# Kernel optimization log

Measured on AMD Instinct MI355X. Metric: run time of the kernel, lower is better.

The kernel has to match this reference:

```python
import jax, jax.numpy as jnp
import numpy as np

D = 1024
H = 4
HD = D // H
WIN = 128
NPMEM = 4
EPS = 1e-5


def _layernorm(x, g, b):
    mu = jnp.mean(x, axis=-1, keepdims=True)
    var = jnp.var(x, axis=-1, keepdims=True)
    return (x - mu) * jax.lax.rsqrt(var + EPS) * g + b


def _rotate_half(t):
    h = t.shape[-1] // 2
    return jnp.concatenate([-t[..., h:], t[..., :h]], axis=-1)


def setup_inputs() -> dict:
    key = jax.random.key(0)
    ks = jax.random.split(key, 20)
    B, L = 2, 4096
    s = 0.02
    inp = {
        'x': jax.random.normal(ks[0], (B, L, D), jnp.float32),
        'cos': jax.random.uniform(ks[1], (L + 8, HD), jnp.float32),
        'sin': jax.random.uniform(ks[2], (L + 8, HD), jnp.float32),
        'global_out': jax.random.normal(ks[3], (B, L, D), jnp.float32),
        'local_out': jax.random.normal(ks[4], (B, L, D), jnp.float32),
        'wq': jax.random.normal(ks[5], (D, D), jnp.float32) * s,
        'wk': jax.random.normal(ks[6], (D, D), jnp.float32) * s,
        'wv': jax.random.normal(ks[7], (D, D), jnp.float32) * s,
        'wo_attn': jax.random.normal(ks[8], (D, D), jnp.float32) * s,
        'pmem': jax.random.normal(ks[9], (1, NPMEM, D), jnp.float32),
        'gate_w': jax.random.normal(ks[10], (3 * D, 3 * D), jnp.float32) * s,
        'gate_b': jnp.zeros((3 * D,), jnp.float32),
        'outproj_w': jax.random.normal(ks[11], (3 * D, D), jnp.float32) * s,
        'outproj_b': jnp.zeros((D,), jnp.float32),
        'ln_mem_g': jnp.ones((D,), jnp.float32),
        'ln_mem_b': jnp.zeros((D,), jnp.float32),
        'ln_mlp_g': jnp.ones((D,), jnp.float32),
        'ln_mlp_b': jnp.zeros((D,), jnp.float32),
        'fc1_w': jax.random.normal(ks[12], (D, 4 * D), jnp.float32) * s,
        'fc1_b': jnp.zeros((4 * D,), jnp.float32),
        'fc2_w': jax.random.normal(ks[13], (4 * D, D), jnp.float32) * s,
        'fc2_b': jnp.zeros((D,), jnp.float32),
    }
    return inp


def reference(x, cos, sin, global_out, local_out, wq, wk, wv, wo_attn, pmem,
              gate_w, gate_b, outproj_w, outproj_b, ln_mem_g, ln_mem_b,
              ln_mlp_g, ln_mlp_b, fc1_w, fc1_b, fc2_w, fc2_b):
    B, L, _ = x.shape
    residual = x

    # prepend persistent memory tokens
    xp = jnp.concatenate([jnp.broadcast_to(pmem, (B, NPMEM, D)), x], axis=1)
    Lt = L + NPMEM

    q = (xp @ wq).reshape(B, Lt, H, HD)
    k = (xp @ wk).reshape(B, Lt, H, HD)
    v = (xp @ wv).reshape(B, Lt, H, HD)

    # rotary embedding over the full pmem+seq length
    cc = cos[:Lt][None, :, None, :]
    ss = sin[:Lt][None, :, None, :]
    q = q * cc + _rotate_half(q) * ss
    k = k * cc + _rotate_half(k) * ss

    i = jnp.arange(Lt)[:, None]
    j = jnp.arange(Lt)[None, :]
    mask = (j <= i) & (j >= i - WIN)  # [Lt, Lt]

    scale = 1.0 / jnp.sqrt(jnp.asarray(HD, x.dtype))
    scores = jnp.einsum('blhd,bmhd->bhlm', q, k) * scale
    scores = jnp.where(mask[None, None], scores, jnp.finfo(scores.dtype).min)
    attn = jax.nn.softmax(scores, axis=-1)
    out = jnp.einsum('bhlm,bmhd->blhd', attn, v).reshape(B, Lt, D)
    core_out = (out @ wo_attn)[:, -L:, :]

    combined = jnp.concatenate([global_out, local_out, core_out], axis=-1)
    g = jax.nn.sigmoid(combined @ gate_w + gate_b)
    memory_output = (combined * g) @ outproj_w + outproj_b

    x1 = residual + _layernorm(memory_output, ln_mem_g, ln_mem_b)
    xn = _layernorm(x1, ln_mlp_g, ln_mlp_b)
    mlp_out = jax.nn.silu(xn @ fc1_w + fc1_b) @ fc2_w + fc2_b
    return x1 + mlp_out
```

## Files before the change

kernel.cpp:

```cpp
#include <hip/hip_runtime.h>
#include <stdint.h>

#define D_    1024
#define H_    4
#define HD_   256
#define WIN_  128
#define NPM_  4
#define B_    2
#define L_    4096
#define LT_   4100
#define LTP_  4112
#define QKL_  3072

typedef __attribute__((ext_vector_type(8))) short short8;
typedef __attribute__((ext_vector_type(4))) float f32x4;

__device__ __forceinline__ short f2bf(float f) {
  union { float f; uint32_t u; } v; v.f = f;
  uint32_t r = v.u + 0x7FFFu + ((v.u >> 16) & 1u);
  return (short)(r >> 16);
}
__device__ __forceinline__ float bf2f(short h) {
  union { uint32_t u; float f; } v; v.u = ((uint32_t)(uint16_t)h) << 16;
  return v.f;
}

#define EP_BF16 0
#define EP_F32B 1
#define EP_GATE 2
#define EP_SILU 3
#define EP_RES  4
#define EP_CORE 5

template<int EP, int TM>
__global__ __launch_bounds__(256, 2)
void gemm_bt(const short* __restrict__ A, int lda,
             const short* __restrict__ Bt,
             void* __restrict__ Cp, int ldc,
             const float* __restrict__ bias,
             const void* __restrict__ aux, int ldaux,
             int M, int N, int K)
{
  constexpr int WM = TM / 2;
  constexpr int MT = WM / 16;
  constexpr int BUFSZ = (TM + 128) * 32;
  __shared__ __attribute__((aligned(16))) short lds[2 * BUFSZ];
  const int tid  = threadIdx.x;
  const int lane = tid & 63, wave = tid >> 6;
  const int lhi  = lane >> 4, llo = lane & 15;
  const int m0 = blockIdx.x * TM, n0 = blockIdx.y * 128;
  const int mw = (wave >> 1) * WM, nw = (wave & 1) * 64;

  const int srow = tid >> 2;
  const int sg   = (tid & 3) ^ ((tid >> 3) & 3);
  const short* pA0 = A + (size_t)min(m0 + srow, M - 1) * lda + sg * 8;
  const short* pA1 = (TM == 128) ? A + (size_t)min(m0 + srow + 64, M - 1) * lda + sg * 8 : pA0;
  const short* pB0 = Bt + (size_t)(n0 + srow) * K + sg * 8;
  const short* pB1 = Bt + (size_t)(n0 + srow + 64) * K + sg * 8;

  const int segoff = (lhi ^ ((llo >> 1) & 3)) * 8;

  short8 ra0, ra1, rb0, rb1;
  auto loadk = [&](int k) {
    ra0 = *(const short8*)(pA0 + k);
    if constexpr (TM == 128) ra1 = *(const short8*)(pA1 + k);
    rb0 = *(const short8*)(pB0 + k);
    rb1 = *(const short8*)(pB1 + k);
  };
  auto stage = [&](int b) {
    short* base = &lds[b * BUFSZ];
    *(short8*)&base[tid * 8] = ra0;
    if constexpr (TM == 128) *(short8*)&base[2048 + tid * 8] = ra1;
    *(short8*)&base[TM * 32 + tid * 8]        = rb0;
    *(short8*)&base[TM * 32 + 2048 + tid * 8] = rb1;
  };

  f32x4 acc[MT][4];
#pragma unroll
  for (int i = 0; i < MT; i++)
#pragma unroll
    for (int j = 0; j < 4; j++) acc[i][j] = f32x4{0.f, 0.f, 0.f, 0.f};

  const int NI = K >> 5;
  loadk(0);
  stage(0);
  loadk(32);
  __syncthreads();

  for (int i = 0; i < NI; i++) {
    if (i + 1 < NI) stage((i + 1) & 1);
    if (i + 2 < NI) loadk((i + 2) << 5);
    const short* bufp = &lds[(i & 1) * BUFSZ];
    short8 af[MT], bfr[4];
#pragma unroll
    for (int mt = 0; mt < MT; mt++)
      af[mt] = *(const short8*)&bufp[(mw + mt * 16 + llo) * 32 + segoff];
#pragma unroll
    for (int nt = 0; nt < 4; nt++)
      bfr[nt] = *(const short8*)&bufp[TM * 32 + (nw + nt * 16 + llo) * 32 + segoff];
#pragma unroll
    for (int mt = 0; mt < MT; mt++)
#pragma unroll
      for (int nt = 0; nt < 4; nt++)
        acc[mt][nt] = __builtin_amdgcn_mfma_f32_16x16x32_bf16(af[mt], bfr[nt], acc[mt][nt], 0, 0, 0);
    __syncthreads();
  }

  const int gcb = n0 + nw;
#pragma unroll
  for (int mt = 0; mt < MT; mt++) {
    const int gr0 = m0 + mw + mt * 16 + lhi * 4;
#pragma unroll
    for (int nt = 0; nt < 4; nt++) {
      const int gc = gcb + nt * 16 + llo;
      float bv = 0.f;
      if constexpr (EP != EP_BF16 && EP != EP_CORE) bv = bias[gc];
#pragma unroll
      for (int r = 0; r < 4; r++) {
        const int gr = gr0 + r;
        if (gr >= M) continue;
        const float v = acc[mt][nt][r];
        if constexpr (EP == EP_CORE) {
          const int b   = gr >= LT_ ? 1 : 0;
          const int tok = gr - b * LT_;
          if (tok >= NPM_) {
            const int cr = b * L_ + (tok - NPM_);
            ((short*)Cp)[(size_t)cr * ldc + gc] = f2bf(v);
          }
          continue;
        }
        const size_t idx = (size_t)gr * ldc + gc;
        if constexpr (EP == EP_BF16) {
          ((short*)Cp)[idx] = f2bf(v);
        } else if constexpr (EP == EP_F32B) {
          ((float*)Cp)[idx] = v + bv;
        } else if constexpr (EP == EP_GATE) {
          float g  = 1.f / (1.f + __expf(-(v + bv)));
          float cv = bf2f(((const short*)aux)[(size_t)gr * ldaux + gc]);
          ((short*)Cp)[idx] = f2bf(cv * g);
        } else if constexpr (EP == EP_SILU) {
          float xx = v + bv;
          ((short*)Cp)[idx] = f2bf(xx / (1.f + __expf(-xx)));
        } else {
          ((float*)Cp)[idx] = v + bv + ((const float*)aux)[(size_t)gr * ldaux + gc];
        }
      }
    }
  }
}

struct TAll {
  const float* src[8];
  short* dst[8];
  int C[8];
  int R[8];
  int nbx[8];
  int start[8];
};

__global__ __launch_bounds__(256)
void transpose_all(TAll t)
{
  __shared__ short tile[32][33];
  const int bid = blockIdx.x;
  int w = 0;
#pragma unroll
  for (int i = 1; i < 8; i++) w = (bid >= t.start[i]) ? i : w;
  const int rel = bid - t.start[w];
  const int nbx = t.nbx[w];
  const int bx = rel % nbx, by = rel / nbx;
  const float* src = t.src[w];
  short* dst = t.dst[w];
  const int ld_in = t.C[w], ld_out = t.R[w];
  const int r0 = by * 32, c0 = bx * 32;
  const int tx = threadIdx.x & 31, ty = threadIdx.x >> 5;
#pragma unroll
  for (int i = 0; i < 4; i++)
    tile[ty + i * 8][tx] = f2bf(src[(size_t)(r0 + ty + i * 8) * ld_in + c0 + tx]);
  __syncthreads();
#pragma unroll
  for (int i = 0; i < 4; i++)
    dst[(size_t)(c0 + ty + i * 8) * ld_out + r0 + tx] = tile[tx][ty + i * 8];
}

template<typename Tin>
__global__ __launch_bounds__(256)
void cast_transpose(const Tin* __restrict__ in, short* __restrict__ outp,
                    int R, int C, int ld_in, int ld_out,
                    int zdiv, size_t inA, size_t inB, size_t outA, size_t outB)
{
  __shared__ short tile[32][33];
  const int z = blockIdx.z;
  const Tin* src = in + (size_t)(z / zdiv) * inA + (size_t)(z % zdiv) * inB;
  short* dst = outp + (size_t)(z / zdiv) * outA + (size_t)(z % zdiv) * outB;
  const int r0 = blockIdx.y * 32, c0 = blockIdx.x * 32;
  const int tx = threadIdx.x & 31, ty = threadIdx.x >> 5;
#pragma unroll
  for (int i = 0; i < 4; i++) {
    int r = r0 + ty + i * 8, c = c0 + tx;
    short v = 0;
    if (r < R && c < C) {
      if constexpr (sizeof(Tin) == 4) v = f2bf((float)src[(size_t)r * ld_in + c]);
      else                            v = (short)src[(size_t)r * ld_in + c];
    }
    tile[ty + i * 8][tx] = v;
  }
  __syncthreads();
#pragma unroll
  for (int i = 0; i < 4; i++) {
    int c = c0 + ty + i * 8, r = r0 + tx;
    if (c < C && r < R) dst[(size_t)c * ld_out + r] = tile[tx][ty + i * 8];
  }
}

__global__ __launch_bounds__(256)
void build_xp_k(const float* __restrict__ x, const float* __restrict__ pmem,
                short* __restrict__ xp)
{
  int gid = blockIdx.x * 256 + threadIdx.x;
  int row = gid >> 8;
  int c4  = (gid & 255) * 4;
  int b   = row >= LT_ ? 1 : 0;
  int tok = row - b * LT_;
  const float* src = (tok < NPM_) ? (pmem + (size_t)tok * D_ + c4)
                                  : (x + ((size_t)b * L_ + tok - NPM_) * D_ + c4);
  float4 v = *(const float4*)src;
  short o[4] = {f2bf(v.x), f2bf(v.y), f2bf(v.z), f2bf(v.w)};
  *(short4*)&xp[(size_t)row * D_ + c4] = *(short4*)o;
}

__global__ __launch_bounds__(256)
void combined01_k(const float* __restrict__ go, const float* __restrict__ lo,
                  short* __restrict__ comb)
{
  int gid = blockIdx.x * 256 + threadIdx.x;
  int row = gid >> 9;
  int c4  = (gid & 511) * 4;
  const float* src = (c4 < D_) ? (go + (size_t)row * D_ + c4)
                               : (lo + (size_t)row * D_ + (c4 - D_));
  float4 v = *(const float4*)src;
  short o[4] = {f2bf(v.x), f2bf(v.y), f2bf(v.z), f2bf(v.w)};
  *(short4*)&comb[(size_t)row * 3072 + c4] = *(short4*)o;
}

__global__ __launch_bounds__(256)
void rope_kernel(short* __restrict__ qkv,
                 const float* __restrict__ cosp, const float* __restrict__ sinp)
{
  int gid = blockIdx.x * 256 + threadIdx.x;
  int d   = (gid & 31) * 4;
  int h   = (gid >> 5) & 3;
  int row = gid >> 7;
  int t   = row >= LT_ ? row - LT_ : row;
  size_t base = (size_t)row * QKL_ + h * HD_ + d;
  float4 cl = *(const float4*)&cosp[(size_t)t * HD_ + d];
  float4 ch = *(const float4*)&cosp[(size_t)t * HD_ + d + 128];
  float4 sl = *(const float4*)&sinp[(size_t)t * HD_ + d];
  float4 sh = *(const float4*)&sinp[(size_t)t * HD_ + d + 128];
  short4 ql4 = *(const short4*)&qkv[base],        qh4 = *(const short4*)&qkv[base + 128];
  short4 kl4 = *(const short4*)&qkv[base + 1024], kh4 = *(const short4*)&qkv[base + 1152];
  const float SC = 1.f / 16.f;
  short oql[4], oqh[4], okl[4], okh[4];
#pragma unroll
  for (int j = 0; j < 4; j++) {
    float c0 = ((float*)&cl)[j], c1 = ((float*)&ch)[j];
    float s0 = ((float*)&sl)[j], s1 = ((float*)&sh)[j];
    float ql = bf2f(((short*)&ql4)[j]), qh = bf2f(((short*)&qh4)[j]);
    float kl = bf2f(((short*)&kl4)[j]), kh = bf2f(((short*)&kh4)[j]);
    oql[j] = f2bf((ql * c0 - qh * s0) * SC);
    oqh[j] = f2bf((qh * c1 + ql * s1) * SC);
    okl[j] = f2bf(kl * c0 - kh * s0);
    okh[j] = f2bf(kh * c1 + kl * s1);
  }
  *(short4*)&qkv[base]        = *(short4*)oql;
  *(short4*)&qkv[base + 128]  = *(short4*)oqh;
  *(short4*)&qkv[base + 1024] = *(short4*)okl;
  *(short4*)&qkv[base + 1152] = *(short4*)okh;
}

__global__ __launch_bounds__(256, 1)
void attn_kernel(const short* __restrict__ qkv, const short* __restrict__ vT,
                 short* __restrict__ outp)
{
  __shared__ short lKV[256 * 72];
  __shared__ short lP[64 * 200];
  const int tid  = threadIdx.x;
  const int lane = tid & 63, wave = tid >> 6;
  const int lhi  = lane >> 4, llo = lane & 15;
  const int i0 = blockIdx.x * 64;
  const int h = blockIdx.y, b = blockIdx.z;
  const int kw0 = i0 - 128;
  const size_t vbase = (size_t)(b * H_ + h) * HD_ * LTP_;

  short8 qf[8];
  {
    int ic = min(i0 + wave * 16 + llo, LT_ - 1);
    const short* qrow = qkv + (size_t)(b * LT_ + ic) * QKL_ + h * HD_;
#pragma unroll
    for (int ks = 0; ks < 8; ks++)
      qf[ks] = *(const short8*)(qrow + ks * 32 + lhi * 8);
  }

  f32x4 S[12];
#pragma unroll
  for (int st = 0; st < 12; st++) S[st] = f32x4{0.f, 0.f, 0.f, 0.f};

  for (int kc = 0; kc < 3; kc++) {
    if (kc) __syncthreads();
    {
      int row = tid >> 2;
      int jc = min(max(kw0 + kc * 64 + row, 0), LT_ - 1);
      const short* krow = qkv + (size_t)(b * LT_ + jc) * QKL_ + 1024 + h * HD_;
#pragma unroll
      for (int it = 0; it < 8; it++) {
        int seg = (tid & 3) + it * 4;
        *(short8*)&lKV[row * 264 + seg * 8] = *(const short8*)(krow + seg * 8);
      }
    }
    __syncthreads();
#pragma unroll
    for (int ks = 0; ks < 8; ks++) {
#pragma unroll
      for (int nt = 0; nt < 4; nt++) {
        short8 bf = *(const short8*)&lKV[(nt * 16 + llo) * 264 + ks * 32 + lhi * 8];
        S[kc * 4 + nt] = __builtin_amdgcn_mfma_f32_16x16x32_bf16(qf[ks], bf, S[kc * 4 + nt], 0, 0, 0);
      }
    }
  }

  const int irow = i0 + wave * 16 + lhi * 4;
  float mx[4], sm[4];
#pragma unroll
  for (int r = 0; r < 4; r++) mx[r] = -3.0e38f;
#pragma unroll
  for (int st = 0; st < 12; st++) {
    int j = kw0 + st * 16 + llo;
#pragma unroll
    for (int r = 0; r < 4; r++) {
      int i = irow + r;
      bool ok = (j >= 0) & (j <= i) & (j >= i - WIN_);
      float s = ok ? S[st][r] : -1.0e30f;
      S[st][r] = s;
      mx[r] = fmaxf(mx[r], s);
    }
  }
#pragma unroll
  for (int r = 0; r < 4; r++)
#pragma unroll
    for (int o = 1; o < 16; o <<= 1) mx[r] = fmaxf(mx[r], __shfl_xor(mx[r], o));
#pragma unroll
  for (int r = 0; r < 4; r++) sm[r] = 0.f;
#pragma unroll
  for (int st = 0; st < 12; st++)
#pragma unroll
    for (int r = 0; r < 4; r++) {
      float e = __expf(S[st][r] - mx[r]);
      S[st][r] = e;
      sm[r] += e;
    }
#pragma unroll
  for (int r = 0; r < 4; r++) {
#pragma unroll
    for (int o = 1; o < 16; o <<= 1) sm[r] += __shfl_xor(sm[r], o);
    sm[r] = 1.f / sm[r];
  }

#pragma unroll
  for (int st = 0; st < 12; st++)
#pragma unroll
    for (int r = 0; r < 4; r++)
      lP[(wave * 16 + lhi * 4 + r) * 200 + st * 16 + llo] = f2bf(S[st][r] * sm[r]);

  f32x4 O[16];
#pragma unroll
  for (int nt = 0; nt < 16; nt++) O[nt] = f32x4{0.f, 0.f, 0.f, 0.f};

  for (int kc = 0; kc < 3; kc++) {
    __syncthreads();
#pragma unroll
    for (int it = 0; it < 8; it++) {
      int id = it * 256 + tid;
      int d = id >> 3, seg = id & 7;
      int kbase = min(max(kw0 + kc * 64 + seg * 8, 0), LTP_ - 8);
      *(short8*)&lKV[d * 72 + seg * 8] = *(const short8*)&vT[vbase + (size_t)d * LTP_ + kbase];
    }
    __syncthreads();
#pragma unroll
    for (int ks = 0; ks < 2; ks++) {
      short8 pf = *(const short8*)&lP[(wave * 16 + llo) * 200 + kc * 64 + ks * 32 + lhi * 8];
#pragma unroll
      for (int nt = 0; nt < 16; nt++) {
        short8 vf = *(const short8*)&lKV[(nt * 16 + llo) * 72 + ks * 32 + lhi * 8];
        O[nt] = __builtin_amdgcn_mfma_f32_16x16x32_bf16(pf, vf, O[nt], 0, 0, 0);
      }
    }
  }

  short* orow = outp + (size_t)(b * LT_) * D_ + h * HD_;
#pragma unroll
  for (int nt = 0; nt < 16; nt++)
#pragma unroll
    for (int r = 0; r < 4; r++) {
      int i = irow + r;
      if (i < LT_) orow[(size_t)i * D_ + nt * 16 + llo] = f2bf(O[nt][r]);
    }
}

__global__ __launch_bounds__(256, 4)
void ln2_kernel(const float* __restrict__ mo, const float* __restrict__ xres,
                const float* __restrict__ g1, const float* __restrict__ b1,
                const float* __restrict__ g2, const float* __restrict__ b2,
                float* __restrict__ x1, short* __restrict__ xn)
{
  const int row = blockIdx.x;
  const int tid = threadIdx.x;
  const int lane = tid & 63, wave = tid >> 6;
  __shared__ float red[8], red2[8];
  float4 v = ((const float4*)(mo + (size_t)row * D_))[tid];
  float s = v.x + v.y + v.z + v.w;
  float s2 = v.x * v.x + v.y * v.y + v.z * v.z + v.w * v.w;
#pragma unroll
  for (int o = 1; o < 64; o <<= 1) { s += __shfl_xor(s, o); s2 += __shfl_xor(s2, o); }
  if (lane == 0) { red[wave] = s; red[wave + 4] = s2; }
  __syncthreads();
  float S = red[0] + red[1] + red[2] + red[3];
  float S2 = red[4] + red[5] + red[6] + red[7];
  float mu = S * (1.f / D_);
  float rs = rsqrtf(S2 * (1.f / D_) - mu * mu + 1e-5f);
  float4 gg = ((const float4*)g1)[tid];
  float4 bb = ((const float4*)b1)[tid];
  float4 xv = ((const float4*)(xres + (size_t)row * D_))[tid];
  float4 o1;
  o1.x = xv.x + (v.x - mu) * rs * gg.x + bb.x;
  o1.y = xv.y + (v.y - mu) * rs * gg.y + bb.y;
  o1.z = xv.z + (v.z - mu) * rs * gg.z + bb.z;
  o1.w = xv.w + (v.w - mu) * rs * gg.w + bb.w;
  ((float4*)(x1 + (size_t)row * D_))[tid] = o1;
  s = o1.x + o1.y + o1.z + o1.w;
  s2 = o1.x * o1.x + o1.y * o1.y + o1.z * o1.z + o1.w * o1.w;
#pragma unroll
  for (int o = 1; o < 64; o <<= 1) { s += __shfl_xor(s, o); s2 += __shfl_xor(s2, o); }
  if (lane == 0) { red2[wave] = s; red2[wave + 4] = s2; }
  __syncthreads();
  S = red2[0] + red2[1] + red2[2] + red2[3];
  S2 = red2[4] + red2[5] + red2[6] + red2[7];
  float mu2 = S * (1.f / D_);
  float rs2 = rsqrtf(S2 * (1.f / D_) - mu2 * mu2 + 1e-5f);
  float4 g2v = ((const float4*)g2)[tid];
  float4 b2v = ((const float4*)b2)[tid];
  short o2[4];
  o2[0] = f2bf((o1.x - mu2) * rs2 * g2v.x + b2v.x);
  o2[1] = f2bf((o1.y - mu2) * rs2 * g2v.y + b2v.y);
  o2[2] = f2bf((o1.z - mu2) * rs2 * g2v.z + b2v.z);
  o2[3] = f2bf((o1.w - mu2) * rs2 * g2v.w + b2v.w);
  *(short4*)&xn[(size_t)row * D_ + tid * 4] = *(short4*)o2;
}

extern "C" void kernel_launch(void* const* d_in, const int* in_sizes, int n_in,
                              void* d_out, int out_size, void* d_ws, size_t ws_size,
                              hipStream_t stream)
{
  const float* x      = (const float*)d_in[0];
  const float* cosp   = (const float*)d_in[1];
  const float* sinp   = (const float*)d_in[2];
  const float* go     = (const float*)d_in[3];
  const float* lo     = (const float*)d_in[4];
  const float* wq     = (const float*)d_in[5];
  const float* wk     = (const float*)d_in[6];
  const float* wv     = (const float*)d_in[7];
  const float* wo     = (const float*)d_in[8];
  const float* pmem   = (const float*)d_in[9];
  const float* gate_w = (const float*)d_in[10];
  const float* gate_b = (const float*)d_in[11];
  const float* outp_w = (const float*)d_in[12];
  const float* outp_b = (const float*)d_in[13];
  const float* ln1g   = (const float*)d_in[14];
  const float* ln1b   = (const float*)d_in[15];
  const float* ln2g   = (const float*)d_in[16];
  const float* ln2b   = (const float*)d_in[17];
  const float* fc1w   = (const float*)d_in[18];
  const float* fc1b   = (const float*)d_in[19];
  const float* fc2w   = (const float*)d_in[20];
  const float* fc2b   = (const float*)d_in[21];
  float* out = (float*)d_out;
  char* p = (char*)d_ws;

  short* wqkvT = (short*)(p + 0);
  short* woT   = (short*)(p + 6291456);
  short* gateT = (short*)(p + 8388608);
  short* outpT = (short*)(p + 27262976);
  short* fc1T  = (short*)(p + 33554432);
  short* fc2T  = (short*)(p + 41943040);
  short* comb  = (short*)(p + 50331648);
  char*  pool  = p + 100663296;
  short* xp    = (short*)(pool);
  short* qkv   = (short*)(pool + 16793600);
  short* vT    = (short*)(pool + 67174400);
  short* a_o   = (short*)(pool + 84017152);
  short* gated = (short*)(pool);
  short* h1    = (short*)(pool);
  float* mo    = (float*)(pool + 67174400);
  float* x1    = (float*)(comb);
  short* xn    = (short*)((char*)comb + 33554432);

  TAll t;
  const float* srcs[8] = {wq, wk, wv, wo, gate_w, outp_w, fc1w, fc2w};
  short* dsts[8] = {wqkvT, wqkvT + 1048576, wqkvT + 2097152, woT, gateT, outpT, fc1T, fc2T};
  const int Rs[8] = {1024, 1024, 1024, 1024, 3072, 3072, 1024, 4096};
  const int Cs[8] = {1024, 1024, 1024, 1024, 3072, 1024, 4096, 1024};
  int cum = 0;
  for (int i = 0; i < 8; i++) {
    t.src[i] = srcs[i]; t.dst[i] = dsts[i];
    t.R[i] = Rs[i]; t.C[i] = Cs[i]; t.nbx[i] = Cs[i] / 32;
    t.start[i] = cum;
    cum += (Cs[i] / 32) * (Rs[i] / 32);
  }
  transpose_all<<<cum, 256, 0, stream>>>(t);

  build_xp_k<<<8200, 256, 0, stream>>>(x, pmem, xp);
  combined01_k<<<16384, 256, 0, stream>>>(go, lo, comb);

  const int Mq = B_ * LT_;
  gemm_bt<EP_BF16, 128><<<dim3(65, 24), 256, 0, stream>>>(xp, 1024, wqkvT, qkv, QKL_, nullptr, nullptr, 0, Mq, 3072, 1024);

  rope_kernel<<<4100, 256, 0, stream>>>(qkv, cosp, sinp);
  cast_transpose<short><<<dim3(8, 129, 8), 256, 0, stream>>>(
      qkv + 2048, vT, LT_, 256, QKL_, LTP_, 4,
      (size_t)LT_ * QKL_, 256, (size_t)4 * 256 * LTP_, (size_t)256 * LTP_);

  attn_kernel<<<dim3(65, H_, B_), 256, 0, stream>>>(qkv, vT, a_o);

  gemm_bt<EP_CORE, 64><<<dim3(129, 8), 256, 0, stream>>>(
      a_o, 1024, woT, comb + 2048, 3072, nullptr, nullptr, 0, Mq, 1024, 1024);

  gemm_bt<EP_GATE, 128><<<dim3(64, 24), 256, 0, stream>>>(comb, 3072, gateT, gated, 3072, gate_b, comb, 3072, 8192, 3072, 3072);

  gemm_bt<EP_F32B, 64><<<dim3(128, 8), 256, 0, stream>>>(gated, 3072, outpT, mo, 1024, outp_b, nullptr, 0, 8192, 1024, 3072);

  ln2_kernel<<<8192, 256, 0, stream>>>(mo, x, ln1g, ln1b, ln2g, ln2b, x1, xn);

  gemm_bt<EP_SILU, 128><<<dim3(64, 32), 256, 0, stream>>>(xn, 1024, fc1T, h1, 4096, fc1b, nullptr, 0, 8192, 4096, 1024);
  gemm_bt<EP_RES, 64><<<dim3(128, 8), 256, 0, stream>>>(h1, 4096, fc2T, out, 1024, fc2b, x1, 1024, 8192, 1024, 4096);
}
```

Measured before the change: 985.7 us.

## Replace GEMMs with 256x256-tile kernel using direct global-to-LDS loads

```diff
diff --git a/kernel.cpp b/kernel.cpp
--- a/kernel.cpp
+++ b/kernel.cpp
@@ -24,6 +24,16 @@
   union { uint32_t u; float f; } v; v.u = ((uint32_t)(uint16_t)h) << 16;
   return v.f;
 }
+
+typedef __attribute__((address_space(1))) void GAS;
+typedef __attribute__((address_space(3))) void LAS;
+__device__ __forceinline__ void gl16(const void* g, void* l) {
+  __builtin_amdgcn_global_load_lds((GAS*)g, (LAS*)l, 16, 0, 0);
+}
+__device__ __forceinline__ void waitvm8() { asm volatile("s_waitcnt vmcnt(8)" ::: "memory"); }
+__device__ __forceinline__ void waitvm4() { asm volatile("s_waitcnt vmcnt(4)" ::: "memory"); }
+__device__ __forceinline__ void waitvm0() { asm volatile("s_waitcnt vmcnt(0)" ::: "memory"); }
+__device__ __forceinline__ void waitlg0() { asm volatile("s_waitcnt lgkmcnt(0)" ::: "memory"); }
 
 #define EP_BF16 0
 #define EP_F32B 1
@@ -149,6 +159,171 @@
   }
 }
 
+template<int EP>
+__global__ __launch_bounds__(512, 2)
+void gemm_bt256(const short* __restrict__ A,
+                const short* __restrict__ Bt,
+                void* __restrict__ Cp, int ldc,
+                const float* __restrict__ bias,
+                const void* __restrict__ aux, int ldaux,
+                int M, int N, int K)
+{
+  __shared__ __attribute__((aligned(128))) short lds[65536];
+  const int tid  = threadIdx.x;
+  const int lane = tid & 63, wave = tid >> 6;
+  const int llo  = lane & 15, lhi = lane >> 4;
+  const int wm = wave >> 2, wn = wave & 3;
+  const int m0 = blockIdx.x * 256, n0 = blockIdx.y * 256;
+
+  const int s0   = wave * 128 + lane;
+  const int srow = s0 >> 2;
+  const int kd   = ((s0 & 3) ^ (srow & 3) ^ ((srow >> 2) & 3)) * 8;
+  const short* aS0 = A  + (size_t)min(m0 + srow,      M - 1) * K + kd;
+  const short* aS1 = A  + (size_t)min(m0 + srow + 16, M - 1) * K + kd;
+  const short* bS0 = Bt + (size_t)(n0 + srow) * K + kd;
+  const short* bS1 = Bt + (size_t)(n0 + srow + 16) * K + kd;
+  const int ld0 = (wave * 128 + lane) * 16;
+  const int ld1 = ld0 + 1024;
+
+  auto stageA = [&](int kt, int h) {
+    const int ko = kt * 64 + h * 32;
+    char* d = (char*)lds + (kt & 1) * 65536 + h * 16384;
+    gl16(aS0 + ko, d + ld0);
+    gl16(aS1 + ko, d + ld1);
+  };
+  auto stageB = [&](int kt, int h) {
+    const int ko = kt * 64 + h * 32;
+    char* d = (char*)lds + (kt & 1) * 65536 + 32768 + h * 16384;
+    gl16(bS0 + ko, d + ld0);
+    gl16(bS1 + ko, d + ld1);
+  };
+
+  int aoff[8], boff[4];
+#pragma unroll
+  for (int mf = 0; mf < 8; mf++) {
+    const int row = wm * 128 + mf * 16 + llo;
+    aoff[mf] = row * 64 + ((lhi ^ (row & 3) ^ ((row >> 2) & 3)) * 16);
+  }
+#pragma unroll
+  for (int nf = 0; nf < 4; nf++) {
+    const int row = wn * 64 + nf * 16 + llo;
+    boff[nf] = row * 64 + ((lhi ^ (row & 3) ^ ((row >> 2) & 3)) * 16);
+  }
+
+  f32x4 acc[8][4];
+#pragma unroll
+  for (int i = 0; i < 8; i++)
+#pragma unroll
+    for (int j = 0; j < 4; j++) acc[i][j] = f32x4{0.f, 0.f, 0.f, 0.f};
+
+  short8 af[4], bfr[4];
+  auto loadA4 = [&](int buf, int ks, int hf) {
+    const char* base = (const char*)lds + buf * 65536 + ks * 16384;
+#pragma unroll
+    for (int i = 0; i < 4; i++) af[i] = *(const short8*)(base + aoff[hf * 4 + i]);
+  };
+  auto loadB4 = [&](int buf, int ks) {
+    const char* base = (const char*)lds + buf * 65536 + 32768 + ks * 16384;
+#pragma unroll
+    for (int i = 0; i < 4; i++) bfr[i] = *(const short8*)(base + boff[i]);
+  };
+
+  const int NT = K >> 6;
+
+  stageA(0, 0); stageB(0, 0); stageA(0, 1); stageB(0, 1);
+  if (NT > 1) { stageA(1, 0); stageB(1, 0); waitvm8(); }
+  else        { waitvm0(); }
+  __builtin_amdgcn_sched_barrier(0);
+  __builtin_amdgcn_s_barrier();
+
+  for (int t = 0; t < NT; ++t) {
+    const int buf = t & 1;
+
+#define PHASE_MFMA(HF)                                                         \
+    __builtin_amdgcn_s_barrier();                                              \
+    waitlg0();                                                                 \
+    __builtin_amdgcn_sched_barrier(0);                                         \
+    __builtin_amdgcn_s_setprio(1);                                             \
+    _Pragma("unroll")                                                          \
+    for (int i = 0; i < 4; i++) {                                              \
+      _Pragma("unroll")                                                        \
+      for (int nf = 0; nf < 4; nf++)                                           \
+        acc[(HF) * 4 + i][nf] = __builtin_amdgcn_mfma_f32_16x16x32_bf16(       \
+            af[i], bfr[nf], acc[(HF) * 4 + i][nf], 0, 0, 0);                   \
+    }                                                                          \
+    __builtin_amdgcn_s_setprio(0);
+
+    loadA4(buf, 0, 0); loadB4(buf, 0);
+    if (t + 1 < NT) stageA(t + 1, 1);
+    PHASE_MFMA(0)
+    __builtin_amdgcn_s_barrier();
+
+    loadA4(buf, 0, 1);
+    if (t + 1 < NT) stageB(t + 1, 1);
+    PHASE_MFMA(1)
+    if (t + 1 < NT) waitvm8(); else waitvm0();
+    __builtin_amdgcn_sched_barrier(0);
+    __builtin_amdgcn_s_barrier();
+
+    loadA4(buf, 1, 0); loadB4(buf, 1);
+    if (t + 2 < NT) stageA(t + 2, 0);
+    PHASE_MFMA(0)
+    __builtin_amdgcn_s_barrier();
+
+    loadA4(buf, 1, 1);
+    if (t + 2 < NT) stageB(t + 2, 0);
+    PHASE_MFMA(1)
+    if (t + 2 < NT) {
+      waitvm8(); __builtin_amdgcn_sched_barrier(0); __builtin_amdgcn_s_barrier();
+    } else if (t + 1 < NT) {
+      waitvm4(); __builtin_amdgcn_sched_barrier(0); __builtin_amdgcn_s_barrier();
+    }
+#undef PHASE_MFMA
+  }
+
+  const int gcb = n0 + wn * 64;
+#pragma unroll
+  for (int mf = 0; mf < 8; mf++) {
+    const int gr0 = m0 + wm * 128 + mf * 16 + lhi * 4;
+#pragma unroll
+    for (int nt = 0; nt < 4; nt++) {
+      const int gc = gcb + nt * 16 + llo;
+      float bv = 0.f;
+      if constexpr (EP != EP_BF16 && EP != EP_CORE) bv = bias[gc];
+#pragma unroll
+      for (int r = 0; r < 4; r++) {
+        const int gr = gr0 + r;
+        if (gr >= M) continue;
+        const float v = acc[mf][nt][r];
+        if constexpr (EP == EP_CORE) {
+          const int b   = gr >= LT_ ? 1 : 0;
+          const int tok = gr - b * LT_;
+          if (tok >= NPM_) {
+            const int cr = b * L_ + (tok - NPM_);
+            ((short*)Cp)[(size_t)cr * ldc + gc] = f2bf(v);
+          }
+          continue;
+        }
+        const size_t idx = (size_t)gr * ldc + gc;
+        if constexpr (EP == EP_BF16) {
+          ((short*)Cp)[idx] = f2bf(v);
+        } else if constexpr (EP == EP_F32B) {
+          ((float*)Cp)[idx] = v + bv;
+        } else if constexpr (EP == EP_GATE) {
+          float g  = 1.f / (1.f + __expf(-(v + bv)));
+          float cv = bf2f(((const short*)aux)[(size_t)gr * ldaux + gc]);
+          ((short*)Cp)[idx] = f2bf(cv * g);
+        } else if constexpr (EP == EP_SILU) {
+          float xx = v + bv;
+          ((short*)Cp)[idx] = f2bf(xx / (1.f + __expf(-xx)));
+        } else {
+          ((float*)Cp)[idx] = v + bv + ((const float*)aux)[(size_t)gr * ldaux + gc];
+        }
+      }
+    }
+  }
+}
+
 struct TAll {
   const float* src[8];
   short* dst[8];
@@ -521,7 +696,7 @@
   combined01_k<<<16384, 256, 0, stream>>>(go, lo, comb);
 
   const int Mq = B_ * LT_;
-  gemm_bt<EP_BF16, 128><<<dim3(65, 24), 256, 0, stream>>>(xp, 1024, wqkvT, qkv, QKL_, nullptr, nullptr, 0, Mq, 3072, 1024);
+  gemm_bt256<EP_BF16><<<dim3(33, 12), 512, 0, stream>>>(xp, wqkvT, qkv, QKL_, nullptr, nullptr, 0, Mq, 3072, 1024);
 
   rope_kernel<<<4100, 256, 0, stream>>>(qkv, cosp, sinp);
   cast_transpose<short><<<dim3(8, 129, 8), 256, 0, stream>>>(
@@ -530,15 +705,15 @@
 
   attn_kernel<<<dim3(65, H_, B_), 256, 0, stream>>>(qkv, vT, a_o);
 
-  gemm_bt<EP_CORE, 64><<<dim3(129, 8), 256, 0, stream>>>(
-      a_o, 1024, woT, comb + 2048, 3072, nullptr, nullptr, 0, Mq, 1024, 1024);
-
-  gemm_bt<EP_GATE, 128><<<dim3(64, 24), 256, 0, stream>>>(comb, 3072, gateT, gated, 3072, gate_b, comb, 3072, 8192, 3072, 3072);
-
-  gemm_bt<EP_F32B, 64><<<dim3(128, 8), 256, 0, stream>>>(gated, 3072, outpT, mo, 1024, outp_b, nullptr, 0, 8192, 1024, 3072);
+  gemm_bt256<EP_CORE><<<dim3(33, 4), 512, 0, stream>>>(
+      a_o, woT, comb + 2048, 3072, nullptr, nullptr, 0, Mq, 1024, 1024);
+
+  gemm_bt256<EP_GATE><<<dim3(32, 12), 512, 0, stream>>>(comb, gateT, gated, 3072, gate_b, comb, 3072, 8192, 3072, 3072);
+
+  gemm_bt256<EP_F32B><<<dim3(32, 4), 512, 0, stream>>>(gated, outpT, mo, 1024, outp_b, nullptr, 0, 8192, 1024, 3072);
 
   ln2_kernel<<<8192, 256, 0, stream>>>(mo, x, ln1g, ln1b, ln2g, ln2b, x1, xn);
 
-  gemm_bt<EP_SILU, 128><<<dim3(64, 32), 256, 0, stream>>>(xn, 1024, fc1T, h1, 4096, fc1b, nullptr, 0, 8192, 4096, 1024);
-  gemm_bt<EP_RES, 64><<<dim3(128, 8), 256, 0, stream>>>(h1, 4096, fc2T, out, 1024, fc2b, x1, 1024, 8192, 1024, 4096);
-}
+  gemm_bt256<EP_SILU><<<dim3(32, 16), 512, 0, stream>>>(xn, fc1T, h1, 4096, fc1b, nullptr, 0, 8192, 4096, 1024);
+  gemm_bt256<EP_RES><<<dim3(32, 4), 512, 0, stream>>>(h1, fc2T, out, 1024, fc2b, x1, 1024, 8192, 1024, 4096);
+}
```

Measured after the change: 1.066 ms. +8.2%, slower.

## Use direct global-to-LDS loads with a four-buffer pipeline in GEMM

Applied to the files above, without the earlier changes.

```diff
diff --git a/kernel.cpp b/kernel.cpp
--- a/kernel.cpp
+++ b/kernel.cpp
@@ -25,6 +25,19 @@
   return v.f;
 }
 
+typedef __attribute__((address_space(1))) void GAS;
+typedef __attribute__((address_space(3))) void LAS;
+__device__ __forceinline__ void gl16(const void* g, void* l) {
+  __builtin_amdgcn_global_load_lds((GAS*)g, (LAS*)l, 16, 0, 0);
+}
+template<int N> __device__ __forceinline__ void waitvmN() {
+  if constexpr (N == 8)      asm volatile("s_waitcnt vmcnt(8)" ::: "memory");
+  else if constexpr (N == 6) asm volatile("s_waitcnt vmcnt(6)" ::: "memory");
+  else if constexpr (N == 4) asm volatile("s_waitcnt vmcnt(4)" ::: "memory");
+  else if constexpr (N == 3) asm volatile("s_waitcnt vmcnt(3)" ::: "memory");
+  else                       asm volatile("s_waitcnt vmcnt(0)" ::: "memory");
+}
+
 #define EP_BF16 0
 #define EP_F32B 1
 #define EP_GATE 2
@@ -44,7 +57,8 @@
   constexpr int WM = TM / 2;
   constexpr int MT = WM / 16;
   constexpr int BUFSZ = (TM + 128) * 32;
-  __shared__ __attribute__((aligned(16))) short lds[2 * BUFSZ];
+  constexpr int G = (TM == 128) ? 4 : 3;
+  __shared__ __attribute__((aligned(16))) short lds[4 * BUFSZ];
   const int tid  = threadIdx.x;
   const int lane = tid & 63, wave = tid >> 6;
   const int lhi  = lane >> 4, llo = lane & 15;
@@ -60,20 +74,14 @@
 
   const int segoff = (lhi ^ ((llo >> 1) & 3)) * 8;
 
-  short8 ra0, ra1, rb0, rb1;
-  auto loadk = [&](int k) {
-    ra0 = *(const short8*)(pA0 + k);
-    if constexpr (TM == 128) ra1 = *(const short8*)(pA1 + k);
-    rb0 = *(const short8*)(pB0 + k);
-    rb1 = *(const short8*)(pB1 + k);
+  auto stage = [&](int b, int i) {
+    const int k = i << 5;
+    short* base = &lds[b * BUFSZ];
+    gl16(pA0 + k, &base[tid * 8]);
+    if constexpr (TM == 128) gl16(pA1 + k, &base[2048 + tid * 8]);
+    gl16(pB0 + k, &base[TM * 32 + tid * 8]);
+    gl16(pB1 + k, &base[TM * 32 + 2048 + tid * 8]);
   };
-  auto stage = [&](int b) {
-    short* base = &lds[b * BUFSZ];
-    *(short8*)&base[tid * 8] = ra0;
-    if constexpr (TM == 128) *(short8*)&base[2048 + tid * 8] = ra1;
-    *(short8*)&base[TM * 32 + tid * 8]        = rb0;
-    *(short8*)&base[TM * 32 + 2048 + tid * 8] = rb1;
-  };
 
   f32x4 acc[MT][4];
 #pragma unroll
@@ -82,15 +90,16 @@
     for (int j = 0; j < 4; j++) acc[i][j] = f32x4{0.f, 0.f, 0.f, 0.f};
 
   const int NI = K >> 5;
-  loadk(0);
-  stage(0);
-  loadk(32);
-  __syncthreads();
+  stage(0, 0);
+  if (NI > 1) stage(1, 1);
 
   for (int i = 0; i < NI; i++) {
-    if (i + 1 < NI) stage((i + 1) & 1);
-    if (i + 2 < NI) loadk((i + 2) << 5);
-    const short* bufp = &lds[(i & 1) * BUFSZ];
+    if (i + 2 < NI) { stage((i + 2) & 3, i + 2); waitvmN<2 * G>(); }
+    else if (i + 1 < NI) waitvmN<G>();
+    else waitvmN<0>();
+    __builtin_amdgcn_s_barrier();
+    __builtin_amdgcn_sched_barrier(0);
+    const short* bufp = &lds[(i & 3) * BUFSZ];
     short8 af[MT], bfr[4];
 #pragma unroll
     for (int mt = 0; mt < MT; mt++)
@@ -103,7 +112,6 @@
 #pragma unroll
       for (int nt = 0; nt < 4; nt++)
         acc[mt][nt] = __builtin_amdgcn_mfma_f32_16x16x32_bf16(af[mt], bfr[nt], acc[mt][nt], 0, 0, 0);
-    __syncthreads();
   }
 
   const int gcb = n0 + nw;
```

Result: slower. 1.049 ms (+6.4%).
